# Kernel optimization log

Hardware: AMD Instinct MI355X
Metric: run time of the kernel (lower is better)

## Reference

```python
import jax, jax.numpy as jnp
import numpy as np

N_EMBD = 384
HEAD_SIZE = 16

def setup_inputs() -> dict:
    key = jax.random.key(0)
    k1, k2, k3, k4 = jax.random.split(key, 4)
    B, T = 4, 4096
    x = jax.random.normal(k1, (B, T, N_EMBD), dtype=jnp.float32)
    # nn.Linear(n_embd, head_size, bias=False): y = x @ W^T, W: [head_size, n_embd].
    # Store transposed [n_embd, head_size] for direct matmul.
    s = 1.0 / np.sqrt(N_EMBD)
    Wk = jax.random.uniform(k2, (N_EMBD, HEAD_SIZE), jnp.float32, -s, s)
    Wq = jax.random.uniform(k3, (N_EMBD, HEAD_SIZE), jnp.float32, -s, s)
    Wv = jax.random.uniform(k4, (N_EMBD, HEAD_SIZE), jnp.float32, -s, s)
    return {"x": x, "Wk": Wk, "Wq": Wq, "Wv": Wv}

def reference(x, Wk, Wq, Wv):
    B, T, C = x.shape
    k = x @ Wk  # [B,T,H]
    q = x @ Wq
    v = x @ Wv
    scale = k.shape[-1] ** -0.5
    wei = jnp.einsum('bth,bsh->bts', q, k) * scale  # [B,T,T]
    causal = jnp.tril(jnp.ones((T, T), dtype=bool))
    wei = jnp.where(causal, wei, -jnp.inf)
    wei = jax.nn.softmax(wei, axis=-1)
    out = jnp.einsum('bts,bsh->bth', wei, v)  # [B,T,H]
    return out
```

## Files before the change

### kernel.cpp

```cpp
#include <hip/hip_runtime.h>


constexpr int B_DIM = 4;
constexpr int T_SEQ = 4096;
constexpr int C_DIM = 384;
constexpr int H_DIM = 16;
constexpr int NROW  = B_DIM * T_SEQ;

typedef __bf16 bf16x8 __attribute__((ext_vector_type(8)));
typedef float  f32x4  __attribute__((ext_vector_type(4)));

__device__ __forceinline__ unsigned short f2bf(float f) {
  unsigned int u = __builtin_bit_cast(unsigned int, f);
  u += 0x7fffu + ((u >> 16) & 1u);
  return (unsigned short)(u >> 16);
}
__device__ __forceinline__ bf16x8 as_bf16x8(uint4 u) {
  return __builtin_bit_cast(bf16x8, u);
}
__device__ __forceinline__ unsigned cvt_pk_bf16(float lo, float hi) {
  unsigned r;
  asm("v_cvt_pk_bf16_f32 %0, %1, %2" : "=v"(r) : "v"(lo), "v"(hi));
  return r;
}

__global__ __launch_bounds__(256) void wconv(
    const float* __restrict__ Wk, const float* __restrict__ Wq,
    const float* __restrict__ Wv, unsigned short* __restrict__ WT) {
  const int i = blockIdx.x * 256 + threadIdx.x;
  const int m = i / 6144;
  const int r = i - m * 6144;
  const int n = r / 384;
  const int k = r - n * 384;
  const float* __restrict__ W = (m == 0) ? Wk : (m == 1) ? Wq : Wv;
  WT[i] = f2bf(W[k * 16 + n]);
}

__global__ __launch_bounds__(128) void qkv_mfma(
    const float* __restrict__ x, const unsigned short* __restrict__ WT,
    unsigned short* __restrict__ Kb,
    unsigned short* __restrict__ Qb,
    unsigned short* __restrict__ VTb)
{
  const int tid  = threadIdx.x;
  const int w    = tid >> 6;
  const int lane = tid & 63;
  const int quad = lane >> 4;
  const int col  = lane & 15;
  const int r0   = blockIdx.x << 4;
  const int kb   = w * 6;

  __shared__ float mrg[12][64];

  const float4* __restrict__ xp =
      reinterpret_cast<const float4*>(x + (size_t)(r0 + col) * C_DIM) + quad * 2;
  float4 araw[12];
#pragma unroll
  for (int kk = 0; kk < 6; ++kk) {
    araw[2 * kk]     = xp[(kb + kk) * 8];
    araw[2 * kk + 1] = xp[(kb + kk) * 8 + 1];
  }

  const uint4* __restrict__ bk = reinterpret_cast<const uint4*>(
      WT + (size_t)col * 384 + quad * 8);
  const uint4* __restrict__ bq = bk + 768;
  const uint4* __restrict__ bv = bk + 1536;

  f32x4 ck = {0.f, 0.f, 0.f, 0.f};
  f32x4 cq = {0.f, 0.f, 0.f, 0.f};
  f32x4 cv = {0.f, 0.f, 0.f, 0.f};
#pragma unroll
  for (int kk = 0; kk < 6; ++kk) {
    uint4 pk;
    const float4 a0 = araw[2 * kk], a1 = araw[2 * kk + 1];
    pk.x = cvt_pk_bf16(a0.x, a0.y);
    pk.y = cvt_pk_bf16(a0.z, a0.w);
    pk.z = cvt_pk_bf16(a1.x, a1.y);
    pk.w = cvt_pk_bf16(a1.z, a1.w);
    const bf16x8 av = as_bf16x8(pk);
    ck = __builtin_amdgcn_mfma_f32_16x16x32_bf16(av, as_bf16x8(bk[(kb + kk) * 4]), ck, 0, 0, 0);
    cq = __builtin_amdgcn_mfma_f32_16x16x32_bf16(av, as_bf16x8(bq[(kb + kk) * 4]), cq, 0, 0, 0);
    cv = __builtin_amdgcn_mfma_f32_16x16x32_bf16(av, as_bf16x8(bv[(kb + kk) * 4]), cv, 0, 0, 0);
  }

  if (w == 1) {
#pragma unroll
    for (int r = 0; r < 4; ++r) {
      mrg[r][lane]     = ck[r];
      mrg[4 + r][lane] = cq[r];
      mrg[8 + r][lane] = cv[r];
    }
  }
  __syncthreads();
  if (w == 0) {
    const float SC = 0.25f * 1.44269504088896341f;
#pragma unroll
    for (int r = 0; r < 4; ++r) {
      const float vk = ck[r] + mrg[r][lane];
      const float vq = cq[r] + mrg[4 + r][lane];
      const float vv = cv[r] + mrg[8 + r][lane];
      const int row = r0 + quad * 4 + r;
      Kb[row * 16 + col]      = f2bf(vk);
      Qb[row * 32 + col]      = f2bf(vq * SC);
      Qb[row * 32 + 16 + col] = 0;
      const int bb = row >> 12, t = row & 4095;
      VTb[(((size_t)(bb * 16 + col)) << 12) + t] = f2bf(vv);
    }
  }
}

__global__ __launch_bounds__(256) void flash_v5(
    const unsigned short* __restrict__ Qb,
    const unsigned short* __restrict__ Kb,
    const unsigned short* __restrict__ VTb,
    float* __restrict__ PO, float* __restrict__ PL)
{
  const int tid  = threadIdx.x;
  const int w    = tid >> 6;
  const int lane = tid & 63;
  const int quad = lane >> 4;
  const int col  = lane & 15;
  const int qt   = 255 - (blockIdx.x >> 3);
  const int b    = (blockIdx.x >> 1) & 3;
  const int h    = blockIdx.x & 1;
  const int slot = h * 4 + w;
  const int r0   = qt << 4;

  __shared__ __attribute__((aligned(16))) unsigned short Pl[4][2][16 * 72];

  const uint4* qp = reinterpret_cast<const uint4*>(
      Qb + (((size_t)(b * T_SEQ + r0 + col)) << 5) + quad * 8);
  const bf16x8 qa = as_bf16x8(qp[0]);

  f32x4 o = {0.f, 0.f, 0.f, 0.f};
  float l4[4] = {0.f, 0.f, 0.f, 0.f};

  const unsigned short* Kbase = Kb + ((size_t)(b * T_SEQ) << 4);
  const unsigned short* Vbase = VTb + (((size_t)(b * 16 + col)) << 12);
  const int nch = (qt + 4) >> 2;
  const int poff = col * 72 + quad * 4;

  unsigned short* const P0 = Pl[w][0];
  unsigned short* const P1 = Pl[w][1];

  auto computeP = [&](int c, unsigned short* P) {
    const int kt0 = c << 2;
    f32x4 sf[4];
#pragma unroll
    for (int t = 0; t < 4; ++t) {
      const int kt = kt0 + t;
      if (kt <= qt) {
        const uint4* kp = reinterpret_cast<const uint4*>(
            Kbase + (((size_t)(kt * 16 + col)) << 4) + quad * 8);
        f32x4 z = {0.f, 0.f, 0.f, 0.f};
        sf[t] = __builtin_amdgcn_mfma_f32_16x16x32_bf16(as_bf16x8(kp[0]), qa, z, 0, 0, 0);
      } else {
#pragma unroll
        for (int r = 0; r < 4; ++r) sf[t][r] = -1e30f;
      }
    }
    const int td = qt - kt0;
    if (td >= 0 && td < 4) {
#pragma unroll
      for (int r = 0; r < 4; ++r)
        if (quad * 4 + r > col) sf[td][r] = -1e30f;
    }
#pragma unroll
    for (int t = 0; t < 4; ++t) {
      const float p0 = __builtin_amdgcn_exp2f(sf[t][0]);
      const float p1 = __builtin_amdgcn_exp2f(sf[t][1]);
      const float p2 = __builtin_amdgcn_exp2f(sf[t][2]);
      const float p3 = __builtin_amdgcn_exp2f(sf[t][3]);
      l4[t] += (p0 + p1) + (p2 + p3);
      uint2 pr;
      pr.x = cvt_pk_bf16(p0, p1);
      pr.y = cvt_pk_bf16(p2, p3);
      *reinterpret_cast<uint2*>(P + poff + t * 16) = pr;
    }
  };

  auto doPV = [&](int c, const unsigned short* P) {
    const uint4 v0 = *reinterpret_cast<const uint4*>(Vbase + c * 64 + quad * 8);
    const uint4 v1 = *reinterpret_cast<const uint4*>(Vbase + c * 64 + 32 + quad * 8);
    const uint4 p0 = *reinterpret_cast<const uint4*>(P + col * 72 + quad * 8);
    const uint4 p1 = *reinterpret_cast<const uint4*>(P + col * 72 + 32 + quad * 8);
    o = __builtin_amdgcn_mfma_f32_16x16x32_bf16(as_bf16x8(p0), as_bf16x8(v0), o, 0, 0, 0);
    o = __builtin_amdgcn_mfma_f32_16x16x32_bf16(as_bf16x8(p1), as_bf16x8(v1), o, 0, 0, 0);
  };

  int c = slot;
  if (c < nch) {
    computeP(c, P0);
    int last = c; c += 8;
    while (c < nch) {
      computeP(c, P1);
      doPV(last, P0);
      last = c; c += 8;
      if (c >= nch) { doPV(last, P1); last = -1; break; }
      computeP(c, P0);
      doPV(last, P1);
      last = c; c += 8;
    }
    if (last >= 0) doPV(last, P0);
  }

  float l = (l4[0] + l4[1]) + (l4[2] + l4[3]);
  l += __shfl_xor(l, 16);
  l += __shfl_xor(l, 32);

  const size_t rowbase = (size_t)b * T_SEQ + r0;
  float* pO = PO + ((size_t)slot * NROW + rowbase) * 16;
#pragma unroll
  for (int r = 0; r < 4; ++r)
    pO[(quad * 4 + r) * 16 + col] = o[r];
  if (quad == 0) PL[(size_t)slot * NROW + rowbase + col] = l;
}

__global__ __launch_bounds__(256) void flash_merge(
    const float* __restrict__ PO, const float* __restrict__ PL,
    float* __restrict__ out)
{
  const int i   = blockIdx.x * 256 + threadIdx.x;
  const int row = i >> 4;
  float O = 0.f, L = 0.f;
#pragma unroll
  for (int s = 0; s < 8; ++s) {
    O += PO[((size_t)s * NROW) * 16 + i];
    L += PL[(size_t)s * NROW + row];
  }
  out[i] = O / L;
}

extern "C" void kernel_launch(void* const* d_in, const int* in_sizes, int n_in,
                              void* d_out, int out_size, void* d_ws, size_t ws_size,
                              hipStream_t stream) {
  const float* x  = (const float*)d_in[0];
  const float* Wk = (const float*)d_in[1];
  const float* Wq = (const float*)d_in[2];
  const float* Wv = (const float*)d_in[3];
  float* outp = (float*)d_out;

  unsigned short* Qb  = (unsigned short*)d_ws;
  unsigned short* Kb  = Qb + (size_t)NROW * 32;
  unsigned short* VTb = Kb + (size_t)NROW * 16 + 64;
  unsigned short* WT  = VTb + (size_t)NROW * 16;
  float* PO = (float*)(WT + 18432);
  float* PL = PO + (size_t)8 * NROW * 16;

  wconv<<<72, 256, 0, stream>>>(Wk, Wq, Wv, WT);
  qkv_mfma<<<1024, 128, 0, stream>>>(x, WT, Kb, Qb, VTb);
  flash_v5<<<2048, 256, 0, stream>>>(Qb, Kb, VTb, PO, PL);
  flash_merge<<<1024, 256, 0, stream>>>(PO, PL, outp);
}
```

Baseline: 102.3 us.

## Pair causal query tiles per block to balance work across 16 slots

Each flash block now handles two query tiles, p and 255-p, so every block gets roughly equal causal work. The key-chunk loop runs over one combined index space of 65 chunks, strided across 16 slots (4 blocks × 4 waves) instead of 8. The kernel also gains a launch-bounds occupancy hint. The cost is doubling the partial-output and partial-sum buffers, which increases write and merge-read traffic, plus some extra control logic.

```diff
diff --git a/kernel.cpp b/kernel.cpp
--- a/kernel.cpp
+++ b/kernel.cpp
@@ -6,6 +6,7 @@
 constexpr int C_DIM = 384;
 constexpr int H_DIM = 16;
 constexpr int NROW  = B_DIM * T_SEQ;
+constexpr int NSLOT = 16;
 
 typedef __bf16 bf16x8 __attribute__((ext_vector_type(8)));
 typedef float  f32x4  __attribute__((ext_vector_type(4)));
@@ -109,7 +110,7 @@
   }
 }
 
-__global__ __launch_bounds__(256) void flash_v5(
+__global__ __launch_bounds__(256, 8) void flash_v6(
     const unsigned short* __restrict__ Qb,
     const unsigned short* __restrict__ Kb,
     const unsigned short* __restrict__ VTb,
@@ -120,30 +121,26 @@
   const int lane = tid & 63;
   const int quad = lane >> 4;
   const int col  = lane & 15;
-  const int qt   = 255 - (blockIdx.x >> 3);
-  const int b    = (blockIdx.x >> 1) & 3;
-  const int h    = blockIdx.x & 1;
-  const int slot = h * 4 + w;
-  const int r0   = qt << 4;
+  const int p    = blockIdx.x >> 4;
+  const int b    = (blockIdx.x >> 2) & 3;
+  const int j    = blockIdx.x & 3;
+  const int slot = (j << 2) | w;
+  const int qtA  = 255 - p;
+  const int qtB  = p;
+  const int nchA = (qtA + 4) >> 2;
 
   __shared__ __attribute__((aligned(16))) unsigned short Pl[4][2][16 * 72];
-
-  const uint4* qp = reinterpret_cast<const uint4*>(
-      Qb + (((size_t)(b * T_SEQ + r0 + col)) << 5) + quad * 8);
-  const bf16x8 qa = as_bf16x8(qp[0]);
-
-  f32x4 o = {0.f, 0.f, 0.f, 0.f};
-  float l4[4] = {0.f, 0.f, 0.f, 0.f};
+  unsigned short* const Pb0 = Pl[w][0];
 
   const unsigned short* Kbase = Kb + ((size_t)(b * T_SEQ) << 4);
   const unsigned short* Vbase = VTb + (((size_t)(b * 16 + col)) << 12);
-  const int nch = (qt + 4) >> 2;
   const int poff = col * 72 + quad * 4;
 
-  unsigned short* const P0 = Pl[w][0];
-  unsigned short* const P1 = Pl[w][1];
-
-  auto computeP = [&](int c, unsigned short* P) {
+  f32x4 o = {0.f, 0.f, 0.f, 0.f};
+
+  auto buf = [&](int i) -> unsigned short* { return Pb0 + i * (16 * 72); };
+
+  auto computeP = [&](int qt, bf16x8 qa, int c, unsigned short* P, float& lref) {
     const int kt0 = c << 2;
     f32x4 sf[4];
 #pragma unroll
@@ -154,29 +151,30 @@
             Kbase + (((size_t)(kt * 16 + col)) << 4) + quad * 8);
         f32x4 z = {0.f, 0.f, 0.f, 0.f};
         sf[t] = __builtin_amdgcn_mfma_f32_16x16x32_bf16(as_bf16x8(kp[0]), qa, z, 0, 0, 0);
+        if (kt == qt) {
+#pragma unroll
+          for (int r = 0; r < 4; ++r)
+            if (quad * 4 + r > col) sf[t][r] = -1e30f;
+        }
       } else {
 #pragma unroll
         for (int r = 0; r < 4; ++r) sf[t][r] = -1e30f;
       }
     }
-    const int td = qt - kt0;
-    if (td >= 0 && td < 4) {
-#pragma unroll
-      for (int r = 0; r < 4; ++r)
-        if (quad * 4 + r > col) sf[td][r] = -1e30f;
-    }
+    float lsum = 0.f;
 #pragma unroll
     for (int t = 0; t < 4; ++t) {
       const float p0 = __builtin_amdgcn_exp2f(sf[t][0]);
       const float p1 = __builtin_amdgcn_exp2f(sf[t][1]);
       const float p2 = __builtin_amdgcn_exp2f(sf[t][2]);
       const float p3 = __builtin_amdgcn_exp2f(sf[t][3]);
-      l4[t] += (p0 + p1) + (p2 + p3);
+      lsum += (p0 + p1) + (p2 + p3);
       uint2 pr;
       pr.x = cvt_pk_bf16(p0, p1);
       pr.y = cvt_pk_bf16(p2, p3);
       *reinterpret_cast<uint2*>(P + poff + t * 16) = pr;
     }
+    lref += lsum;
   };
 
   auto doPV = [&](int c, const unsigned short* P) {
@@ -188,32 +186,58 @@
     o = __builtin_amdgcn_mfma_f32_16x16x32_bf16(as_bf16x8(p1), as_bf16x8(v1), o, 0, 0, 0);
   };
 
-  int c = slot;
-  if (c < nch) {
-    computeP(c, P0);
-    int last = c; c += 8;
-    while (c < nch) {
-      computeP(c, P1);
-      doPV(last, P0);
-      last = c; c += 8;
-      if (c >= nch) { doPV(last, P1); last = -1; break; }
-      computeP(c, P0);
-      doPV(last, P1);
-      last = c; c += 8;
-    }
-    if (last >= 0) doPV(last, P0);
-  }
-
-  float l = (l4[0] + l4[1]) + (l4[2] + l4[3]);
-  l += __shfl_xor(l, 16);
-  l += __shfl_xor(l, 32);
-
-  const size_t rowbase = (size_t)b * T_SEQ + r0;
-  float* pO = PO + ((size_t)slot * NROW + rowbase) * 16;
-#pragma unroll
-  for (int r = 0; r < 4; ++r)
-    pO[(quad * 4 + r) * 16 + col] = o[r];
-  if (quad == 0) PL[(size_t)slot * NROW + rowbase + col] = l;
+  auto writePartial = [&](int qt, float lsum) {
+    float l = lsum;
+    l += __shfl_xor(l, 16);
+    l += __shfl_xor(l, 32);
+    const size_t rowbase = (size_t)b * T_SEQ + ((size_t)qt << 4);
+    float* pO = PO + ((size_t)slot * NROW + rowbase) * 16;
+#pragma unroll
+    for (int r = 0; r < 4; ++r)
+      pO[(quad * 4 + r) * 16 + col] = o[r];
+    if (quad == 0) PL[(size_t)slot * NROW + rowbase + col] = l;
+  };
+
+  const uint4* qpA = reinterpret_cast<const uint4*>(
+      Qb + (((size_t)(b * T_SEQ + (qtA << 4) + col)) << 5) + quad * 8);
+  const bf16x8 qaA = as_bf16x8(qpA[0]);
+
+  float lA = 0.f, lB = 0.f;
+  int g = slot;
+  computeP(qtA, qaA, g, buf(0), lA);
+  int prevC = g;
+  int pb = 0;
+  for (g += 16; g < nchA; g += 16) {
+    computeP(qtA, qaA, g, buf(pb ^ 1), lA);
+    doPV(prevC, buf(pb));
+    prevC = g;
+    pb ^= 1;
+  }
+
+  const int gB = g;
+  bf16x8 qaB = qaA;
+  if (gB < 65) {
+    const uint4* qpB = reinterpret_cast<const uint4*>(
+        Qb + (((size_t)(b * T_SEQ + (qtB << 4) + col)) << 5) + quad * 8);
+    qaB = as_bf16x8(qpB[0]);
+    computeP(qtB, qaB, gB - nchA, buf(pb ^ 1), lB);
+  }
+  doPV(prevC, buf(pb));
+  writePartial(qtA, lA);
+  o = (f32x4){0.f, 0.f, 0.f, 0.f};
+
+  if (gB < 65) {
+    pb ^= 1;
+    int prevB = gB - nchA;
+    for (int g2 = gB + 16; g2 < 65; g2 += 16) {
+      computeP(qtB, qaB, g2 - nchA, buf(pb ^ 1), lB);
+      doPV(prevB, buf(pb));
+      prevB = g2 - nchA;
+      pb ^= 1;
+    }
+    doPV(prevB, buf(pb));
+  }
+  writePartial(qtB, lB);
 }
 
 __global__ __launch_bounds__(256) void flash_merge(
@@ -224,7 +248,7 @@
   const int row = i >> 4;
   float O = 0.f, L = 0.f;
 #pragma unroll
-  for (int s = 0; s < 8; ++s) {
+  for (int s = 0; s < NSLOT; ++s) {
     O += PO[((size_t)s * NROW) * 16 + i];
     L += PL[(size_t)s * NROW + row];
   }
@@ -245,10 +269,10 @@
   unsigned short* VTb = Kb + (size_t)NROW * 16 + 64;
   unsigned short* WT  = VTb + (size_t)NROW * 16;
   float* PO = (float*)(WT + 18432);
-  float* PL = PO + (size_t)8 * NROW * 16;
+  float* PL = PO + (size_t)NSLOT * NROW * 16;
 
   wconv<<<72, 256, 0, stream>>>(Wk, Wq, Wv, WT);
   qkv_mfma<<<1024, 128, 0, stream>>>(x, WT, Kb, Qb, VTb);
-  flash_v5<<<2048, 256, 0, stream>>>(Qb, Kb, VTb, PO, PL);
+  flash_v6<<<2048, 256, 0, stream>>>(Qb, Kb, VTb, PO, PL);
   flash_merge<<<1024, 256, 0, stream>>>(PO, PL, outp);
 }
```

After: 104.5 us. +2.2%, slower.
